# Optimization experiments

Measured on AMD Instinct MI355X. Metric: run time of the kernel, lower is better.

Reference implementation:

```python
import jax, jax.numpy as jnp
import numpy as np

N_HEAD = 50000
N_TAIL = 50000
E = 800000
F_IN = 256
D = 64
H = 4
FE = 64
N_ETYPES = 5
NEG_SLOPE = 0.2


def setup_inputs() -> dict:
    key = jax.random.key(0)
    ks = jax.random.split(key, 10)
    head_feature = jax.random.normal(ks[0], (N_HEAD, F_IN), jnp.float32)
    tail_feature = jax.random.normal(ks[1], (N_TAIL, F_IN), jnp.float32)
    head_ind = jax.random.randint(ks[2], (E,), 0, N_HEAD)
    tail_ind = jax.random.randint(ks[3], (E,), 0, N_TAIL)
    edge_list = jnp.stack([head_ind, tail_ind], axis=0)  # [2, E]
    tmp_edge = jax.random.randint(ks[4], (E,), 0, N_ETYPES)
    s = 0.05  # small init scale, mimics uniform(-stdv, stdv)
    W = jax.random.normal(ks[5], (F_IN, D * H), jnp.float32) * s
    W_e = jax.random.normal(ks[6], (FE, FE * H), jnp.float32) * s
    edge_emb = jax.random.normal(ks[7], (N_ETYPES, FE), jnp.float32) * s
    a_l = jax.random.normal(ks[8], (1, H, D), jnp.float32) * s
    a_r = jax.random.normal(jax.random.fold_in(ks[8], 1), (1, H, D), jnp.float32) * s
    a_e = jax.random.normal(ks[9], (1, H, FE), jnp.float32) * s
    return {
        "head_feature": head_feature,
        "tail_feature": tail_feature,
        "edge_list": edge_list,
        "tmp_edge": tmp_edge,
        "W": W,
        "W_e": W_e,
        "edge_emb": edge_emb,
        "a_l": a_l,
        "a_r": a_r,
        "a_e": a_e,
    }


def _layer(head_feature, tail_feature, head_ind, tail_ind, tmp_edge,
           W, W_e, edge_emb, a_l, a_r, a_e):
    n_head = head_feature.shape[0]
    # dense projections (dropout = identity in eval)
    h_head = (head_feature @ W).reshape(-1, H, D)      # [N_h, H, D]
    h_tail = (tail_feature @ W).reshape(-1, H, D)      # [N_t, H, D]
    e = (edge_emb @ W_e).reshape(-1, H, FE)            # [T, H, FE]
    # per-edge attention logits
    h_l = (a_l * h_head).sum(-1)[head_ind]             # [E, H]
    h_r = (a_r * h_tail).sum(-1)[tail_ind]             # [E, H]
    h_e = (a_e * e).sum(-1)[tmp_edge]                  # [E, H]
    score = jax.nn.leaky_relu(h_l + h_r + h_e, NEG_SLOPE)
    # segment softmax over edges grouped by destination (head) node, per head
    m = jax.ops.segment_max(score, head_ind, num_segments=n_head)   # [N_h, H]
    ex = jnp.exp(score - m[head_ind])                               # [E, H]
    z = jax.ops.segment_sum(ex, head_ind, num_segments=n_head)      # [N_h, H]
    alpha = ex / z[head_ind]                                        # [E, H]
    # weighted aggregation: sparse-mm per head, vectorized over heads
    msg = alpha[:, :, None] * h_tail[tail_ind]                      # [E, H, D]
    out = jax.ops.segment_sum(msg, head_ind, num_segments=n_head)   # [N_h, H, D]
    out = out.reshape(n_head, H * D)
    return jax.nn.elu(out)


def reference(head_feature, tail_feature, edge_list, tmp_edge,
              W, W_e, edge_emb, a_l, a_r, a_e):
    head_ind = edge_list[0]
    tail_ind = edge_list[1]
    return _layer(head_feature, tail_feature, head_ind, tail_ind, tmp_edge,
                  W, W_e, edge_emb, a_l, a_r, a_e)
```

## Files before the change

kernel.cpp:

```cpp
#include <hip/hip_runtime.h>
#include <hip/hip_bf16.h>
#include <math.h>

#define N_HEADN 50000
#define N_TAILN 50000
#define NE      800000
#define F_IN    256
#define HH      4
#define HD      256
#define FE      64
#define N_ETYPES 5
#define NEG_SLOPE 0.2f
#define NB_SCAN ((N_HEADN + 255) / 256)
#define NB_CVT  ((N_TAILN * F_IN) / (256 * 16))
#define NB_HIST (NE / 256)
#define NT_PROJ (N_TAILN / 16)
#define NB_PROJ 256

typedef __attribute__((ext_vector_type(8))) short bf16x8;
typedef __attribute__((ext_vector_type(4))) float f32x4;

static __device__ __forceinline__ unsigned short f2bf(float f) {
    unsigned u = __float_as_uint(f);
    return (unsigned short)((u + 0x7FFF + ((u >> 16) & 1)) >> 16);
}
static __device__ __forceinline__ float bf2f(unsigned short u) {
    return __uint_as_float((unsigned)u << 16);
}

__global__ __launch_bounds__(256) void prep_kernel(const int* __restrict__ head,
                                                   int* __restrict__ counts,
                                                   const float* __restrict__ X,
                                                   unsigned short* __restrict__ Xb,
                                                   const float* __restrict__ W,
                                                   const float* __restrict__ a_l,
                                                   const float* __restrict__ W_e,
                                                   const float* __restrict__ a_e,
                                                   const float* __restrict__ edge_emb,
                                                   float* __restrict__ waT,
                                                   float* __restrict__ heo,
                                                   short* __restrict__ Wt) {
    const int b = blockIdx.x;
    if (b < NB_HIST) {
        int e = b * 256 + threadIdx.x;
        atomicAdd(&counts[head[e]], 1);
    } else if (b < NB_HIST + NB_CVT) {
        size_t t = (size_t)(b - NB_HIST) * 256 + threadIdx.x;
        const float4* xp = (const float4*)X + t * 4;
        float4 v0 = xp[0], v1 = xp[1], v2 = xp[2], v3 = xp[3];
        bf16x8 o0, o1;
        o0[0] = (short)f2bf(v0.x); o0[1] = (short)f2bf(v0.y);
        o0[2] = (short)f2bf(v0.z); o0[3] = (short)f2bf(v0.w);
        o0[4] = (short)f2bf(v1.x); o0[5] = (short)f2bf(v1.y);
        o0[6] = (short)f2bf(v1.z); o0[7] = (short)f2bf(v1.w);
        o1[0] = (short)f2bf(v2.x); o1[1] = (short)f2bf(v2.y);
        o1[2] = (short)f2bf(v2.z); o1[3] = (short)f2bf(v2.w);
        o1[4] = (short)f2bf(v3.x); o1[5] = (short)f2bf(v3.y);
        o1[6] = (short)f2bf(v3.z); o1[7] = (short)f2bf(v3.w);
        bf16x8* op = (bf16x8*)(Xb + t * 16);
        op[0] = o0;
        op[1] = o1;
    } else if (b == NB_HIST + NB_CVT) {
        int k = threadIdx.x;
        #pragma unroll
        for (int h = 0; h < HH; ++h) {
            float s = 0.f;
            for (int d = 0; d < 64; ++d) s += a_l[h * 64 + d] * W[(size_t)k * HD + h * 64 + d];
            waT[h * 256 + k] = s;
        }
    } else if (b == NB_HIST + NB_CVT + 1) {
        __shared__ float wae[FE][HH];
        int t = threadIdx.x;
        int k = t >> 2, h = t & 3;
        float s = 0.f;
        for (int f = 0; f < 64; ++f) s += a_e[h * 64 + f] * W_e[(size_t)k * (FE * HH) + h * 64 + f];
        wae[k][h] = s;
        __syncthreads();
        if (t < N_ETYPES * HH) {
            int ty = t >> 2, hh = t & 3;
            float acc = 0.f;
            for (int kk = 0; kk < FE; ++kk) acc += edge_emb[ty * FE + kk] * wae[kk][hh];
            heo[ty * HH + hh] = acc;
        }
    } else {
        int n = b - (NB_HIST + NB_CVT + 2), k = threadIdx.x;
        Wt[(size_t)n * 256 + k] = (short)f2bf(W[(size_t)k * 256 + n]);
    }
}

__global__ void blocksum_kernel(const int* __restrict__ counts, int* __restrict__ blockSums) {
    __shared__ int s[256];
    int t = threadIdx.x, j = blockIdx.x * 256 + t;
    s[t] = (j < N_HEADN) ? counts[j] : 0;
    __syncthreads();
    for (int off = 128; off > 0; off >>= 1) {
        if (t < off) s[t] += s[t + off];
        __syncthreads();
    }
    if (t == 0) blockSums[blockIdx.x] = s[0];
}

__global__ void rowstart_kernel(const int* __restrict__ counts,
                                const int* __restrict__ blockSums,
                                int* __restrict__ row_start, int* __restrict__ cursor) {
    __shared__ int bs[256];
    __shared__ int s[256];
    int t = threadIdx.x, j = blockIdx.x * 256 + t;
    bs[t] = (t < NB_SCAN) ? blockSums[t] : 0;
    __syncthreads();
    for (int off = 1; off < 256; off <<= 1) {
        int u = (t >= off) ? bs[t - off] : 0;
        __syncthreads();
        bs[t] += u;
        __syncthreads();
    }
    const int blockOffV = (blockIdx.x == 0) ? 0 : bs[blockIdx.x - 1];
    int c = (j < N_HEADN) ? counts[j] : 0;
    s[t] = c;
    __syncthreads();
    for (int off = 1; off < 256; off <<= 1) {
        int u = (t >= off) ? s[t - off] : 0;
        __syncthreads();
        s[t] += u;
        __syncthreads();
    }
    int excl = blockOffV + s[t] - c;
    if (j < N_HEADN) {
        row_start[j] = excl;
        cursor[j]    = excl;
        if (j == N_HEADN - 1) row_start[N_HEADN] = excl + c;
    }
}

__global__ __launch_bounds__(256) void head_dot_kernel(const float* __restrict__ X,
                                                       const float* __restrict__ waT,
                                                       float* __restrict__ hl) {
    const int wave = threadIdx.x >> 6;
    const int lane = threadIdx.x & 63;
    const int n = blockIdx.x * 4 + wave;
    float4 x = ((const float4*)(X + (size_t)n * F_IN))[lane];
    float p[HH];
    #pragma unroll
    for (int h = 0; h < HH; ++h) {
        float4 w = ((const float4*)(waT + h * 256))[lane];
        p[h] = x.x * w.x + x.y * w.y + x.z * w.z + x.w * w.w;
    }
    #pragma unroll
    for (int off = 1; off < 64; off <<= 1) {
        #pragma unroll
        for (int h = 0; h < HH; ++h) p[h] += __shfl_xor(p[h], off);
    }
    if (lane < HH) hl[(size_t)n * HH + lane] = p[lane];
}

struct ProjTileOut { };

static __device__ __forceinline__ void proj_load_xf(const unsigned short* __restrict__ Xb,
                                                    int tile, int l15, int quad,
                                                    bf16x8* xf) {
    const unsigned short* xbase = Xb + (size_t)(tile * 16 + l15) * F_IN + quad * 8;
    #pragma unroll
    for (int kk = 0; kk < 8; ++kk) xf[kk] = *(const bf16x8*)(xbase + kk * 32);
}

static __device__ __forceinline__ void proj_compute(const char* __restrict__ smem,
                                                    const float* __restrict__ a,
                                                    unsigned short* __restrict__ h_out,
                                                    float* __restrict__ hr,
                                                    int tile, int h, int lane,
                                                    const bf16x8* xf) {
    const int quad = lane >> 4;
    const int l15  = lane & 15;
    f32x4 acc[4];
    #pragma unroll
    for (int ct = 0; ct < 4; ++ct) acc[ct] = (f32x4){0.f, 0.f, 0.f, 0.f};

    int colb[4], sw[4];
    #pragma unroll
    for (int ct = 0; ct < 4; ++ct) {
        int col = h * 64 + ct * 16 + l15;
        colb[ct] = col * 512;
        sw[ct]   = col & 31;
    }

    #pragma unroll
    for (int kk = 0; kk < 8; ++kk) {
        #pragma unroll
        for (int ct = 0; ct < 4; ++ct) {
            int addr = colb[ct] + ((((quad + kk * 4)) ^ sw[ct]) << 4);
            bf16x8 wf = *(const bf16x8*)(smem + addr);
            acc[ct] = __builtin_amdgcn_mfma_f32_16x16x32_bf16(wf, xf[kk], acc[ct], 0, 0, 0);
        }
    }

    const int row = tile * 16 + l15;
    float hp = 0.f;
    #pragma unroll
    for (int ct = 0; ct < 4; ++ct) {
        float4 av = *(const float4*)(a + h * 64 + ct * 16 + quad * 4);
        hp += av.x * acc[ct][0] + av.y * acc[ct][1]
            + av.z * acc[ct][2] + av.w * acc[ct][3];
        ushort4 pk;
        pk.x = f2bf(acc[ct][0]); pk.y = f2bf(acc[ct][1]);
        pk.z = f2bf(acc[ct][2]); pk.w = f2bf(acc[ct][3]);
        *(ushort4*)(h_out + (size_t)row * HD + h * 64 + ct * 16 + quad * 4) = pk;
    }
    hp += __shfl_xor(hp, 16);
    hp += __shfl_xor(hp, 32);
    if (lane < 16) hr[(size_t)row * HH + h] = hp;
}

__global__ __launch_bounds__(256) void proj_mfma_kernel(const unsigned short* __restrict__ Xb,
                                                        const short* __restrict__ Wt,
                                                        const float* __restrict__ a,
                                                        unsigned short* __restrict__ h_out,
                                                        float* __restrict__ hr) {
    extern __shared__ char smem[];
    const int h    = threadIdx.x >> 6;
    const int lane = threadIdx.x & 63;
    const int l15  = lane & 15;
    const int quad = lane >> 4;

    int tile = blockIdx.x;
    bf16x8 xfA[8], xfB[8];
    if (tile < NT_PROJ) proj_load_xf(Xb, tile, l15, quad, xfA);

    {
        const int t = threadIdx.x;
        #pragma unroll
        for (int i = 0; i < 32; ++i) {
            int m = i * 256 + t;
            bf16x8 v = *(const bf16x8*)(Wt + (size_t)m * 8);
            int col = m >> 5;
            int c   = m & 31;
            *(bf16x8*)(smem + col * 512 + ((c ^ (col & 31)) << 4)) = v;
        }
    }
    __syncthreads();

    while (tile < NT_PROJ) {
        int nxt = tile + NB_PROJ;
        if (nxt < NT_PROJ) proj_load_xf(Xb, nxt, l15, quad, xfB);
        proj_compute(smem, a, h_out, hr, tile, h, lane, xfA);
        tile = nxt;
        if (tile >= NT_PROJ) break;
        nxt = tile + NB_PROJ;
        if (nxt < NT_PROJ) proj_load_xf(Xb, nxt, l15, quad, xfA);
        proj_compute(smem, a, h_out, hr, tile, h, lane, xfB);
        tile = nxt;
    }
}

__global__ void scatter_kernel(const int* __restrict__ head, const int* __restrict__ tail,
                               const int* __restrict__ etype,
                               const float* __restrict__ hl, const float* __restrict__ hr,
                               const float* __restrict__ he,
                               int* __restrict__ cursor, int* __restrict__ packed,
                               float* __restrict__ exE) {
    int e = blockIdx.x * 256 + threadIdx.x;
    int h0 = head[e];
    int tl = tail[e];
    int ty = etype[e];
    float4 L = *(const float4*)(hl + (size_t)h0 * HH);
    float4 R = *(const float4*)(hr + (size_t)tl * HH);
    float4 T = *(const float4*)(he + ty * HH);
    float s0 = L.x + R.x + T.x;
    float s1 = L.y + R.y + T.y;
    float s2 = L.z + R.z + T.z;
    float s3 = L.w + R.w + T.w;
    s0 = (s0 > 0.f) ? s0 : NEG_SLOPE * s0;
    s1 = (s1 > 0.f) ? s1 : NEG_SLOPE * s1;
    s2 = (s2 > 0.f) ? s2 : NEG_SLOPE * s2;
    s3 = (s3 > 0.f) ? s3 : NEG_SLOPE * s3;
    float w0 = __expf(s0), w1 = __expf(s1), w2 = __expf(s2), w3 = __expf(s3);
    int pos = atomicAdd(&cursor[h0], 1);
    packed[pos] = tl;
    *(float4*)(exE + (size_t)pos * HH) = make_float4(w0, w1, w2, w3);
}

__global__ __launch_bounds__(256) void agg_kernel(const int* __restrict__ row_start,
                                                  const int* __restrict__ packed,
                                                  const float* __restrict__ exE,
                                                  const unsigned short* __restrict__ h_tail,
                                                  float* __restrict__ out) {
    const int wave = threadIdx.x >> 6;
    const int lane = threadIdx.x & 63;
    const int n = blockIdx.x * 4 + wave;
    const int s = row_start[n];
    const int e = row_start[n + 1];
    const int g = lane >> 5;
    const int q = lane & 31;
    const int h = q >> 3;

    float acc[8];
    #pragma unroll
    for (int c = 0; c < 8; ++c) acc[c] = 0.f;
    float z = 0.f;

    for (int base = s; base < e; base += 64) {
        const int cnt = (e - base < 64) ? (e - base) : 64;
        int myidx = 0;
        if (base + lane < e) myidx = packed[base + lane];
        #pragma unroll 8
        for (int i = 0; i < cnt; i += 2) {
            const int j = i + g;
            const int tl = __shfl(myidx, j);
            if (j < cnt) {
                const float w = exE[(size_t)(base + j) * HH + h];
                uint4 u = *(const uint4*)(h_tail + (size_t)tl * HD + q * 8);
                #pragma unroll
                for (int d = 0; d < 4; ++d) {
                    unsigned uu = ((const unsigned*)&u)[d];
                    acc[2 * d]     += w * __uint_as_float(uu << 16);
                    acc[2 * d + 1] += w * __uint_as_float(uu & 0xFFFF0000u);
                }
                z += w;
            }
        }
    }

    #pragma unroll
    for (int c = 0; c < 8; ++c) acc[c] += __shfl_xor(acc[c], 32);
    z += __shfl_xor(z, 32);

    float4 o;
    if (z > 0.f) {
        o.x = acc[4 * g + 0] / z;
        o.y = acc[4 * g + 1] / z;
        o.z = acc[4 * g + 2] / z;
        o.w = acc[4 * g + 3] / z;
        o.x = (o.x > 0.f) ? o.x : expm1f(o.x);
        o.y = (o.y > 0.f) ? o.y : expm1f(o.y);
        o.z = (o.z > 0.f) ? o.z : expm1f(o.z);
        o.w = (o.w > 0.f) ? o.w : expm1f(o.w);
    } else {
        o = make_float4(0.f, 0.f, 0.f, 0.f);
    }
    ((float4*)(out + (size_t)n * HD))[q * 2 + g] = o;
}

extern "C" void kernel_launch(void* const* d_in, const int* in_sizes, int n_in,
                              void* d_out, int out_size, void* d_ws, size_t ws_size,
                              hipStream_t stream) {
    const float* head_feature = (const float*)d_in[0];
    const float* tail_feature = (const float*)d_in[1];
    const int*   edge_list    = (const int*)d_in[2];
    const int*   tmp_edge     = (const int*)d_in[3];
    const float* W            = (const float*)d_in[4];
    const float* W_e          = (const float*)d_in[5];
    const float* edge_emb     = (const float*)d_in[6];
    const float* a_l          = (const float*)d_in[7];
    const float* a_r          = (const float*)d_in[8];
    const float* a_e          = (const float*)d_in[9];
    const int* head_ind = edge_list;
    const int* tail_ind = edge_list + NE;

    char* ws = (char*)d_ws;
    unsigned short* h_tail = (unsigned short*)ws; ws += sizeof(unsigned short) * (size_t)N_TAILN * HD;
    unsigned short* Xb = (unsigned short*)ws;
    float* exE    = (float*)(void*)Xb;
    int*   packed = (int*)(void*)((char*)(void*)Xb + sizeof(float) * (size_t)NE * HH);
    ws += sizeof(unsigned short) * (size_t)N_TAILN * HD;
    short* Wt        = (short*)ws; ws += sizeof(short) * 256 * 256;
    float* hl        = (float*)ws; ws += sizeof(float) * (size_t)N_HEADN * HH;
    float* hr        = (float*)ws; ws += sizeof(float) * (size_t)N_TAILN * HH;
    float* waT       = (float*)ws; ws += sizeof(float) * HH * 256;
    float* he        = (float*)ws; ws += sizeof(float) * 32;
    int*   counts    = (int*)ws;   ws += sizeof(int) * (size_t)N_HEADN;
    int*   row_start = (int*)ws;   ws += sizeof(int) * (size_t)(N_HEADN + 4);
    int*   cursor    = (int*)ws;   ws += sizeof(int) * (size_t)N_HEADN;
    int*   blockSums = (int*)ws;   ws += sizeof(int) * 256;

    hipMemsetAsync(counts, 0, sizeof(int) * (size_t)N_HEADN, stream);

    hipLaunchKernelGGL(prep_kernel, dim3(NB_HIST + NB_CVT + 258), dim3(256), 0, stream,
                       head_ind, counts, tail_feature, Xb,
                       W, a_l, W_e, a_e, edge_emb, waT, he, Wt);

    hipLaunchKernelGGL(blocksum_kernel, dim3(NB_SCAN), dim3(256), 0, stream,
                       counts, blockSums);
    hipLaunchKernelGGL(rowstart_kernel, dim3(NB_SCAN), dim3(256), 0, stream,
                       counts, blockSums, row_start, cursor);

    hipLaunchKernelGGL(head_dot_kernel, dim3(N_HEADN / 4), dim3(256), 0, stream,
                       head_feature, waT, hl);

    static bool lds_attr_set = false;
    if (!lds_attr_set) {
        hipFuncSetAttribute((const void*)proj_mfma_kernel,
                            hipFuncAttributeMaxDynamicSharedMemorySize, 131072);
        lds_attr_set = true;
    }
    hipLaunchKernelGGL(proj_mfma_kernel, dim3(NB_PROJ), dim3(256), 131072, stream,
                       Xb, Wt, a_r, h_tail, hr);

    hipLaunchKernelGGL(scatter_kernel, dim3(NE / 256), dim3(256), 0, stream,
                       head_ind, tail_ind, tmp_edge, hl, hr, he, cursor, packed, exE);

    hipLaunchKernelGGL(agg_kernel, dim3(N_HEADN / 4), dim3(256), 0, stream,
                       row_start, packed, exE, h_tail, (float*)d_out);
}
```

Measured before the change: 332.2 us.

## Fuse scan kernels and head-dot into one kernel; use nontemporal memory ops

Merges the two-pass block-sum/row-start scan and the head-dot projection into a single launch. The scan blocks now coordinate through a global atomic flag with a spin-wait instead of a kernel boundary. Separately, many streaming loads and stores (edge indices, features, exE, output) are switched to nontemporal builtins to reduce cache pollution. The goal is to cut launch overhead and let the scan overlap the head-dot work. The spin barrier relies on all scan blocks being co-resident, which holds here since the scan blocks come first in the grid.

```diff
diff --git a/kernel.cpp b/kernel.cpp
--- a/kernel.cpp
+++ b/kernel.cpp
@@ -14,11 +14,13 @@
 #define NB_SCAN ((N_HEADN + 255) / 256)
 #define NB_CVT  ((N_TAILN * F_IN) / (256 * 16))
 #define NB_HIST (NE / 256)
+#define NB_HD   (N_HEADN / 4)
 #define NT_PROJ (N_TAILN / 16)
 #define NB_PROJ 256
 
 typedef __attribute__((ext_vector_type(8))) short bf16x8;
 typedef __attribute__((ext_vector_type(4))) float f32x4;
+typedef __attribute__((ext_vector_type(4))) unsigned u32x4;
 
 static __device__ __forceinline__ unsigned short f2bf(float f) {
     unsigned u = __float_as_uint(f);
@@ -43,23 +45,26 @@
     const int b = blockIdx.x;
     if (b < NB_HIST) {
         int e = b * 256 + threadIdx.x;
-        atomicAdd(&counts[head[e]], 1);
+        atomicAdd(&counts[__builtin_nontemporal_load(&head[e])], 1);
     } else if (b < NB_HIST + NB_CVT) {
         size_t t = (size_t)(b - NB_HIST) * 256 + threadIdx.x;
-        const float4* xp = (const float4*)X + t * 4;
-        float4 v0 = xp[0], v1 = xp[1], v2 = xp[2], v3 = xp[3];
+        const f32x4* xp = (const f32x4*)X + t * 4;
+        f32x4 v0 = __builtin_nontemporal_load(xp + 0);
+        f32x4 v1 = __builtin_nontemporal_load(xp + 1);
+        f32x4 v2 = __builtin_nontemporal_load(xp + 2);
+        f32x4 v3 = __builtin_nontemporal_load(xp + 3);
         bf16x8 o0, o1;
-        o0[0] = (short)f2bf(v0.x); o0[1] = (short)f2bf(v0.y);
-        o0[2] = (short)f2bf(v0.z); o0[3] = (short)f2bf(v0.w);
-        o0[4] = (short)f2bf(v1.x); o0[5] = (short)f2bf(v1.y);
-        o0[6] = (short)f2bf(v1.z); o0[7] = (short)f2bf(v1.w);
-        o1[0] = (short)f2bf(v2.x); o1[1] = (short)f2bf(v2.y);
-        o1[2] = (short)f2bf(v2.z); o1[3] = (short)f2bf(v2.w);
-        o1[4] = (short)f2bf(v3.x); o1[5] = (short)f2bf(v3.y);
-        o1[6] = (short)f2bf(v3.z); o1[7] = (short)f2bf(v3.w);
+        o0[0] = (short)f2bf(v0[0]); o0[1] = (short)f2bf(v0[1]);
+        o0[2] = (short)f2bf(v0[2]); o0[3] = (short)f2bf(v0[3]);
+        o0[4] = (short)f2bf(v1[0]); o0[5] = (short)f2bf(v1[1]);
+        o0[6] = (short)f2bf(v1[2]); o0[7] = (short)f2bf(v1[3]);
+        o1[0] = (short)f2bf(v2[0]); o1[1] = (short)f2bf(v2[1]);
+        o1[2] = (short)f2bf(v2[2]); o1[3] = (short)f2bf(v2[3]);
+        o1[4] = (short)f2bf(v3[0]); o1[5] = (short)f2bf(v3[1]);
+        o1[6] = (short)f2bf(v3[2]); o1[7] = (short)f2bf(v3[3]);
         bf16x8* op = (bf16x8*)(Xb + t * 16);
-        op[0] = o0;
-        op[1] = o1;
+        __builtin_nontemporal_store(o0, op + 0);
+        __builtin_nontemporal_store(o1, op + 1);
     } else if (b == NB_HIST + NB_CVT) {
         int k = threadIdx.x;
         #pragma unroll
@@ -88,79 +93,79 @@
     }
 }
 
-__global__ void blocksum_kernel(const int* __restrict__ counts, int* __restrict__ blockSums) {
-    __shared__ int s[256];
-    int t = threadIdx.x, j = blockIdx.x * 256 + t;
-    s[t] = (j < N_HEADN) ? counts[j] : 0;
-    __syncthreads();
-    for (int off = 128; off > 0; off >>= 1) {
-        if (t < off) s[t] += s[t + off];
+__global__ __launch_bounds__(256) void mid_kernel(const int* __restrict__ counts,
+                                                  int* __restrict__ blockSums,
+                                                  int* __restrict__ scanflag,
+                                                  int* __restrict__ row_start,
+                                                  int* __restrict__ cursor,
+                                                  const float* __restrict__ X,
+                                                  const float* __restrict__ waT,
+                                                  float* __restrict__ hl) {
+    const int b = blockIdx.x;
+    if (b < NB_SCAN) {
+        __shared__ int s[256];
+        __shared__ int bs[256];
+        const int t = threadIdx.x;
+        const int j = b * 256 + t;
+        const int c = (j < N_HEADN) ? counts[j] : 0;
+        s[t] = c;
         __syncthreads();
-    }
-    if (t == 0) blockSums[blockIdx.x] = s[0];
-}
-
-__global__ void rowstart_kernel(const int* __restrict__ counts,
-                                const int* __restrict__ blockSums,
-                                int* __restrict__ row_start, int* __restrict__ cursor) {
-    __shared__ int bs[256];
-    __shared__ int s[256];
-    int t = threadIdx.x, j = blockIdx.x * 256 + t;
-    bs[t] = (t < NB_SCAN) ? blockSums[t] : 0;
-    __syncthreads();
-    for (int off = 1; off < 256; off <<= 1) {
-        int u = (t >= off) ? bs[t - off] : 0;
+        for (int off = 1; off < 256; off <<= 1) {
+            int u = (t >= off) ? s[t - off] : 0;
+            __syncthreads();
+            s[t] += u;
+            __syncthreads();
+        }
+        if (t == 0) {
+            blockSums[b] = s[255];
+            __threadfence();
+            atomicAdd(scanflag, 1);
+            while (atomicAdd(scanflag, 0) < NB_SCAN) {  }
+        }
         __syncthreads();
-        bs[t] += u;
+        __threadfence();
+        bs[t] = (t < NB_SCAN) ? blockSums[t] : 0;
         __syncthreads();
-    }
-    const int blockOffV = (blockIdx.x == 0) ? 0 : bs[blockIdx.x - 1];
-    int c = (j < N_HEADN) ? counts[j] : 0;
-    s[t] = c;
-    __syncthreads();
-    for (int off = 1; off < 256; off <<= 1) {
-        int u = (t >= off) ? s[t - off] : 0;
-        __syncthreads();
-        s[t] += u;
-        __syncthreads();
-    }
-    int excl = blockOffV + s[t] - c;
-    if (j < N_HEADN) {
-        row_start[j] = excl;
-        cursor[j]    = excl;
-        if (j == N_HEADN - 1) row_start[N_HEADN] = excl + c;
-    }
-}
-
-__global__ __launch_bounds__(256) void head_dot_kernel(const float* __restrict__ X,
-                                                       const float* __restrict__ waT,
-                                                       float* __restrict__ hl) {
-    const int wave = threadIdx.x >> 6;
-    const int lane = threadIdx.x & 63;
-    const int n = blockIdx.x * 4 + wave;
-    float4 x = ((const float4*)(X + (size_t)n * F_IN))[lane];
-    float p[HH];
-    #pragma unroll
-    for (int h = 0; h < HH; ++h) {
-        float4 w = ((const float4*)(waT + h * 256))[lane];
-        p[h] = x.x * w.x + x.y * w.y + x.z * w.z + x.w * w.w;
-    }
-    #pragma unroll
-    for (int off = 1; off < 64; off <<= 1) {
+        for (int off = 1; off < 256; off <<= 1) {
+            int u = (t >= off) ? bs[t - off] : 0;
+            __syncthreads();
+            bs[t] += u;
+            __syncthreads();
+        }
+        const int blockOffV = (b == 0) ? 0 : bs[b - 1];
+        int excl = blockOffV + s[t] - c;
+        if (j < N_HEADN) {
+            row_start[j] = excl;
+            cursor[j]    = excl;
+            if (j == N_HEADN - 1) row_start[N_HEADN] = excl + c;
+        }
+    } else {
+        const int wave = threadIdx.x >> 6;
+        const int lane = threadIdx.x & 63;
+        const int n = (b - NB_SCAN) * 4 + wave;
+        f32x4 x = __builtin_nontemporal_load((const f32x4*)(X + (size_t)n * F_IN) + lane);
+        float p[HH];
         #pragma unroll
-        for (int h = 0; h < HH; ++h) p[h] += __shfl_xor(p[h], off);
-    }
-    if (lane < HH) hl[(size_t)n * HH + lane] = p[lane];
-}
-
-struct ProjTileOut { };
+        for (int h = 0; h < HH; ++h) {
+            f32x4 w = *((const f32x4*)(waT + h * 256) + lane);
+            p[h] = x[0] * w[0] + x[1] * w[1] + x[2] * w[2] + x[3] * w[3];
+        }
+        #pragma unroll
+        for (int off = 1; off < 64; off <<= 1) {
+            #pragma unroll
+            for (int h = 0; h < HH; ++h) p[h] += __shfl_xor(p[h], off);
+        }
+        if (lane < HH) hl[(size_t)n * HH + lane] = p[lane];
+    }
+}
 
 static __device__ __forceinline__ void proj_load_xf(const unsigned short* __restrict__ Xb,
                                                     int tile, int l15, int quad,
                                                     bf16x8* xf) {
     const unsigned short* xbase = Xb + (size_t)(tile * 16 + l15) * F_IN + quad * 8;
     #pragma unroll
-    for (int kk = 0; kk < 8; ++kk) xf[kk] = *(const bf16x8*)(xbase + kk * 32);
+    for (int kk = 0; kk < 8; ++kk)
+        xf[kk] = __builtin_nontemporal_load((const bf16x8*)(xbase + kk * 32));
 }
 
 static __device__ __forceinline__ void proj_compute(const char* __restrict__ smem,
@@ -258,9 +263,9 @@
                                int* __restrict__ cursor, int* __restrict__ packed,
                                float* __restrict__ exE) {
     int e = blockIdx.x * 256 + threadIdx.x;
-    int h0 = head[e];
-    int tl = tail[e];
-    int ty = etype[e];
+    int h0 = __builtin_nontemporal_load(&head[e]);
+    int tl = __builtin_nontemporal_load(&tail[e]);
+    int ty = __builtin_nontemporal_load(&etype[e]);
     float4 L = *(const float4*)(hl + (size_t)h0 * HH);
     float4 R = *(const float4*)(hr + (size_t)tl * HH);
     float4 T = *(const float4*)(he + ty * HH);
@@ -275,7 +280,8 @@
     float w0 = __expf(s0), w1 = __expf(s1), w2 = __expf(s2), w3 = __expf(s3);
     int pos = atomicAdd(&cursor[h0], 1);
     packed[pos] = tl;
-    *(float4*)(exE + (size_t)pos * HH) = make_float4(w0, w1, w2, w3);
+    f32x4 wv = (f32x4){w0, w1, w2, w3};
+    __builtin_nontemporal_store(wv, (f32x4*)(exE + (size_t)pos * HH));
 }
 
 __global__ __launch_bounds__(256) void agg_kernel(const int* __restrict__ row_start,
@@ -300,17 +306,17 @@
     for (int base = s; base < e; base += 64) {
         const int cnt = (e - base < 64) ? (e - base) : 64;
         int myidx = 0;
-        if (base + lane < e) myidx = packed[base + lane];
+        if (base + lane < e) myidx = __builtin_nontemporal_load(&packed[base + lane]);
         #pragma unroll 8
         for (int i = 0; i < cnt; i += 2) {
             const int j = i + g;
             const int tl = __shfl(myidx, j);
             if (j < cnt) {
-                const float w = exE[(size_t)(base + j) * HH + h];
-                uint4 u = *(const uint4*)(h_tail + (size_t)tl * HD + q * 8);
+                const float w = __builtin_nontemporal_load(&exE[(size_t)(base + j) * HH + h]);
+                u32x4 u = *(const u32x4*)(h_tail + (size_t)tl * HD + q * 8);
                 #pragma unroll
                 for (int d = 0; d < 4; ++d) {
-                    unsigned uu = ((const unsigned*)&u)[d];
+                    unsigned uu = u[d];
                     acc[2 * d]     += w * __uint_as_float(uu << 16);
                     acc[2 * d + 1] += w * __uint_as_float(uu & 0xFFFF0000u);
                 }
@@ -323,20 +329,20 @@
     for (int c = 0; c < 8; ++c) acc[c] += __shfl_xor(acc[c], 32);
     z += __shfl_xor(z, 32);
 
-    float4 o;
+    f32x4 o;
     if (z > 0.f) {
-        o.x = acc[4 * g + 0] / z;
-        o.y = acc[4 * g + 1] / z;
-        o.z = acc[4 * g + 2] / z;
-        o.w = acc[4 * g + 3] / z;
-        o.x = (o.x > 0.f) ? o.x : expm1f(o.x);
-        o.y = (o.y > 0.f) ? o.y : expm1f(o.y);
-        o.z = (o.z > 0.f) ? o.z : expm1f(o.z);
-        o.w = (o.w > 0.f) ? o.w : expm1f(o.w);
+        o[0] = acc[4 * g + 0] / z;
+        o[1] = acc[4 * g + 1] / z;
+        o[2] = acc[4 * g + 2] / z;
+        o[3] = acc[4 * g + 3] / z;
+        o[0] = (o[0] > 0.f) ? o[0] : expm1f(o[0]);
+        o[1] = (o[1] > 0.f) ? o[1] : expm1f(o[1]);
+        o[2] = (o[2] > 0.f) ? o[2] : expm1f(o[2]);
+        o[3] = (o[3] > 0.f) ? o[3] : expm1f(o[3]);
     } else {
-        o = make_float4(0.f, 0.f, 0.f, 0.f);
-    }
-    ((float4*)(out + (size_t)n * HD))[q * 2 + g] = o;
+        o = (f32x4){0.f, 0.f, 0.f, 0.f};
+    }
+    __builtin_nontemporal_store(o, (f32x4*)(out + (size_t)n * HD) + (q * 2 + g));
 }
 
 extern "C" void kernel_launch(void* const* d_in, const int* in_sizes, int n_in,
@@ -367,22 +373,19 @@
     float* waT       = (float*)ws; ws += sizeof(float) * HH * 256;
     float* he        = (float*)ws; ws += sizeof(float) * 32;
     int*   counts    = (int*)ws;   ws += sizeof(int) * (size_t)N_HEADN;
+    int*   scanflag  = (int*)ws;   ws += sizeof(int) * 4;
     int*   row_start = (int*)ws;   ws += sizeof(int) * (size_t)(N_HEADN + 4);
     int*   cursor    = (int*)ws;   ws += sizeof(int) * (size_t)N_HEADN;
     int*   blockSums = (int*)ws;   ws += sizeof(int) * 256;
 
-    hipMemsetAsync(counts, 0, sizeof(int) * (size_t)N_HEADN, stream);
+    hipMemsetAsync(counts, 0, sizeof(int) * ((size_t)N_HEADN + 4), stream);
 
     hipLaunchKernelGGL(prep_kernel, dim3(NB_HIST + NB_CVT + 258), dim3(256), 0, stream,
                        head_ind, counts, tail_feature, Xb,
                        W, a_l, W_e, a_e, edge_emb, waT, he, Wt);
 
-    hipLaunchKernelGGL(blocksum_kernel, dim3(NB_SCAN), dim3(256), 0, stream,
-                       counts, blockSums);
-    hipLaunchKernelGGL(rowstart_kernel, dim3(NB_SCAN), dim3(256), 0, stream,
-                       counts, blockSums, row_start, cursor);
-
-    hipLaunchKernelGGL(head_dot_kernel, dim3(N_HEADN / 4), dim3(256), 0, stream,
+    hipLaunchKernelGGL(mid_kernel, dim3(NB_SCAN + NB_HD), dim3(256), 0, stream,
+                       counts, blockSums, scanflag, row_start, cursor,
                        head_feature, waT, hl);
 
     static bool lds_attr_set = false;
```

Measured after the change: 398.0 us. 1.2x slower.
